# Kernel optimization log

Hardware: AMD Instinct MI355X
Metric: run time of the kernel (lower is better)

## Reference

```python
import jax, jax.numpy as jnp
import numpy as np

B, S, H = 2, 1024, 2048          # batch, seq, hidden_size
I = 7168                          # intermediate_size
E = 8                             # num_local_experts
TOPK = 2                          # num_experts_per_tok
R = int(I * H * 0.1 / (I + H))    # delta_low_rank = 159


def setup_inputs() -> dict:
    key = jax.random.key(0)
    ks = jax.random.split(key, 12)
    s = 0.02
    return {
        "hidden_states": jax.random.normal(ks[0], (B, S, H), jnp.float32),
        "gate_w": jax.random.normal(ks[1], (E, H), jnp.float32) * s,
        "W1": jax.random.normal(ks[2], (E, I, H), jnp.float32) * s,
        "W2": jax.random.normal(ks[3], (E, H, I), jnp.float32) * s,
        "W3": jax.random.normal(ks[4], (E, I, H), jnp.float32) * s,
        "U1": jax.random.normal(ks[5], (E, I, R), jnp.float32) * s,
        "V1": jax.random.normal(ks[6], (E, R, H), jnp.float32) * s,
        "U2": jax.random.normal(ks[7], (E, H, R), jnp.float32) * s,
        "V2": jax.random.normal(ks[8], (E, R, I), jnp.float32) * s,
        "U3": jax.random.normal(ks[9], (E, I, R), jnp.float32) * s,
        "V3": jax.random.normal(ks[10], (E, R, H), jnp.float32) * s,
    }


def reference(hidden_states, gate_w, W1, W2, W3, U1, V1, U2, V2, U3, V3):
    b, s, h = hidden_states.shape
    x = hidden_states.reshape(-1, h)                     # [T, H]
    T = x.shape[0]
    router_logits = x @ gate_w.T                          # [T, E]
    probs = jax.nn.softmax(router_logits.astype(jnp.float32), axis=-1)
    rw, sel = jax.lax.top_k(probs, TOPK)                  # [T, k]
    rw = rw / jnp.sum(rw, axis=-1, keepdims=True)
    rw = rw.astype(x.dtype)
    # dense combine weights: zero for unselected experts (same math as gather/scatter)
    comb = jnp.zeros((T, E), x.dtype).at[jnp.arange(T)[:, None], sel].add(rw)
    out = jnp.zeros_like(x)
    for e in range(E):                                    # small fixed expert loop
        up = x @ W3[e].T + (x @ V3[e].T) @ U3[e].T        # [T, I]
        gate = x @ W1[e].T + (x @ V1[e].T) @ U1[e].T      # [T, I]
        hmid = jax.nn.silu(gate) * up                     # [T, I]
        y = hmid @ W2[e].T + (hmid @ V2[e].T) @ U2[e].T   # [T, H]
        out = out + comb[:, e, None] * y
    return out.reshape(b, s, h), router_logits
```

## Files before the change

kernel.cpp:

```cpp
#include <hip/hip_runtime.h>
#include <cstdint>
#include <cstddef>

#define TT 2048
#define HH 2048
#define II 7168
#define EE 8
#define RR 159
#define RPAD 192
#define ROWS 4096

typedef __attribute__((ext_vector_type(8))) short bf16x8;
typedef __attribute__((ext_vector_type(4))) short short4v;
typedef __attribute__((ext_vector_type(4))) float f32x4;

__device__ __forceinline__ unsigned short f2bf(float f) {
  unsigned int u = __float_as_uint(f);
  u += 0x7fffu + ((u >> 16) & 1u);
  return (unsigned short)(u >> 16);
}
__device__ __forceinline__ float bf2f(unsigned short u) {
  return __uint_as_float(((unsigned int)u) << 16);
}
__device__ __forceinline__ bf16x8 zero8() {
  bf16x8 v;
#pragma unroll
  for (int j = 0; j < 8; j++) v[j] = 0;
  return v;
}
__device__ __forceinline__ void gload16(const unsigned short* g, unsigned short* l) {
  __builtin_amdgcn_global_load_lds(
      (const __attribute__((address_space(1))) unsigned int*)g,
      (__attribute__((address_space(3))) unsigned int*)l, 16, 0, 0);
}

__global__ __launch_bounds__(256) void k_f2bf_flat(const float* __restrict__ s,
                                                   unsigned short* __restrict__ d,
                                                   long long n8) {
  long long i = (long long)blockIdx.x * blockDim.x + threadIdx.x;
  long long stride = (long long)gridDim.x * blockDim.x;
  for (; i < n8; i += stride) {
    const float* p = s + i * 8;
    float4 a = *(const float4*)p;
    float4 b = *(const float4*)(p + 4);
    bf16x8 v;
    v[0] = (short)f2bf(a.x); v[1] = (short)f2bf(a.y);
    v[2] = (short)f2bf(a.z); v[3] = (short)f2bf(a.w);
    v[4] = (short)f2bf(b.x); v[5] = (short)f2bf(b.y);
    v[6] = (short)f2bf(b.z); v[7] = (short)f2bf(b.w);
    *(bf16x8*)(d + i * 8) = v;
  }
}

__global__ __launch_bounds__(256) void k_upad(const float* __restrict__ U,
                                              unsigned short* __restrict__ Up, int rows) {
  long long idx = (long long)blockIdx.x * 256 + threadIdx.x;
  long long total = (long long)rows * 24;
  if (idx >= total) return;
  int row = (int)(idx / 24), c8 = (int)(idx % 24);
  unsigned short* dp = Up + (size_t)row * RPAD + c8 * 8;
#pragma unroll
  for (int j = 0; j < 8; j++) {
    int c = c8 * 8 + j;
    dp[j] = (c < RR) ? f2bf(U[(size_t)row * RR + c]) : (unsigned short)0;
  }
}

__global__ __launch_bounds__(256, 2) void k_merge(
    const float* __restrict__ Wf, const unsigned short* __restrict__ Upad,
    const unsigned short* __restrict__ Vb, unsigned short* __restrict__ Wb,
    int M2, int C) {
  int e = blockIdx.z;
  int row0 = blockIdx.y * 128;
  int col0 = blockIdx.x * 128;
  const float* w = Wf + (size_t)e * M2 * C;
  const unsigned short* up = Upad + (size_t)e * M2 * RPAD;
  const unsigned short* vb = Vb + (size_t)e * RR * C;
  unsigned short* wb = Wb + (size_t)e * M2 * C;
  __shared__ unsigned short sbuf[17408];
  unsigned short* Us = sbuf;
  unsigned short* Vt = sbuf + 8192;
  unsigned short* Dl = sbuf;
  int tid = threadIdx.x, lane = tid & 63, wv = tid >> 6;
  int wr = (wv >> 1) * 64, wc = (wv & 1) * 64;
  int rstage = tid >> 3, cg = tid & 7;
  f32x4 acc[4][4];
#pragma unroll
  for (int m = 0; m < 4; m++)
#pragma unroll
    for (int n = 0; n < 4; n++) acc[m][n] = (f32x4){0.f, 0.f, 0.f, 0.f};
  int rl = tid & 15;
  int h8 = (tid >> 4) * 8;
  for (int kt = 0; kt < RPAD; kt += 64) {
#pragma unroll
    for (int p = 0; p < 4; p++) {
      int r = p * 32 + rstage;
      bf16x8 v = *(const bf16x8*)(up + (size_t)(row0 + r) * RPAD + kt + cg * 8);
      *(bf16x8*)&Us[r * 64 + ((cg ^ (r & 7)) * 8)] = v;
    }
#pragma unroll
    for (int rr = 0; rr < 4; rr++) {
      int r = rr * 16 + rl;
      int rg = kt + r;
      bf16x8 v = zero8();
      if (rg < RR) v = *(const bf16x8*)(vb + (size_t)rg * C + col0 + h8);
#pragma unroll
      for (int j = 0; j < 8; j++) Vt[(h8 + j) * 72 + r] = (unsigned short)v[j];
    }
    __syncthreads();
#pragma unroll
    for (int ks = 0; ks < 2; ks++) {
      bf16x8 af[4], bf[4];
#pragma unroll
      for (int m = 0; m < 4; m++) {
        int r = wr + m * 16 + (lane & 15);
        af[m] = *(const bf16x8*)&Us[r * 64 + (((ks * 4 + (lane >> 4)) ^ (r & 7)) * 8)];
      }
#pragma unroll
      for (int n = 0; n < 4; n++) {
        int h = wc + n * 16 + (lane & 15);
        bf[n] = *(const bf16x8*)&Vt[h * 72 + (ks * 4 + (lane >> 4)) * 8];
      }
#pragma unroll
      for (int m = 0; m < 4; m++)
#pragma unroll
        for (int n = 0; n < 4; n++)
          acc[m][n] = __builtin_amdgcn_mfma_f32_16x16x32_bf16(af[m], bf[n], acc[m][n], 0, 0, 0);
    }
    __syncthreads();
  }
#pragma unroll
  for (int m = 0; m < 4; m++) {
#pragma unroll
    for (int r4 = 0; r4 < 4; r4++) {
      int row = wr + m * 16 + (lane >> 4) * 4 + r4;
#pragma unroll
      for (int n = 0; n < 4; n++) {
        int col = wc + n * 16 + (lane & 15);
        Dl[row * 136 + col] = f2bf(acc[m][n][r4]);
      }
    }
  }
  __syncthreads();
  {
    int rr = tid >> 5;
    int c4 = (tid & 31) * 4;
#pragma unroll
    for (int pass = 0; pass < 16; pass++) {
      int row = pass * 8 + rr;
      const float* src = w + (size_t)(row0 + row) * C + col0 + c4;
      float4 a = *(const float4*)src;
      const unsigned short* dl = &Dl[row * 136 + c4];
      short4v o;
      o[0] = (short)f2bf(a.x + bf2f(dl[0]));
      o[1] = (short)f2bf(a.y + bf2f(dl[1]));
      o[2] = (short)f2bf(a.z + bf2f(dl[2]));
      o[3] = (short)f2bf(a.w + bf2f(dl[3]));
      *(short4v*)(wb + (size_t)(row0 + row) * C + col0 + c4) = o;
    }
  }
}

__global__ __launch_bounds__(256) void k_router(
    const float* __restrict__ x, const float* __restrict__ gw,
    float* __restrict__ logits_out, int* __restrict__ sel,
    float* __restrict__ wtok, int* __restrict__ counts,
    unsigned short* __restrict__ xb) {
  int t = blockIdx.x;
  const float* xr = x + (size_t)t * HH;
  int base = threadIdx.x * 8;
  float4 x0 = *(const float4*)(xr + base);
  float4 x1 = *(const float4*)(xr + base + 4);
  {
    bf16x8 v;
    v[0] = (short)f2bf(x0.x); v[1] = (short)f2bf(x0.y);
    v[2] = (short)f2bf(x0.z); v[3] = (short)f2bf(x0.w);
    v[4] = (short)f2bf(x1.x); v[5] = (short)f2bf(x1.y);
    v[6] = (short)f2bf(x1.z); v[7] = (short)f2bf(x1.w);
    *(bf16x8*)(xb + (size_t)t * HH + base) = v;
  }
  float part[EE];
#pragma unroll
  for (int e = 0; e < EE; e++) {
    const float* g = gw + (size_t)e * HH + base;
    float4 g0 = *(const float4*)g;
    float4 g1 = *(const float4*)(g + 4);
    part[e] = x0.x * g0.x + x0.y * g0.y + x0.z * g0.z + x0.w * g0.w +
              x1.x * g1.x + x1.y * g1.y + x1.z * g1.z + x1.w * g1.w;
  }
#pragma unroll
  for (int off = 32; off > 0; off >>= 1)
#pragma unroll
    for (int e = 0; e < EE; e++) part[e] += __shfl_down(part[e], off);
  __shared__ float red[4][EE];
  int w = threadIdx.x >> 6, lane = threadIdx.x & 63;
  if (lane == 0) {
#pragma unroll
    for (int e = 0; e < EE; e++) red[w][e] = part[e];
  }
  __syncthreads();
  if (threadIdx.x == 0) {
    float lg[EE];
    float mx = -1e30f;
#pragma unroll
    for (int e = 0; e < EE; e++) {
      lg[e] = red[0][e] + red[1][e] + red[2][e] + red[3][e];
      logits_out[(size_t)t * EE + e] = lg[e];
      mx = fmaxf(mx, lg[e]);
    }
    float p[EE];
#pragma unroll
    for (int e = 0; e < EE; e++) p[e] = __expf(lg[e] - mx);
    int i0 = 0;
#pragma unroll
    for (int e = 1; e < EE; e++)
      if (lg[e] > lg[i0]) i0 = e;
    int i1 = (i0 == 0) ? 1 : 0;
#pragma unroll
    for (int e = 0; e < EE; e++)
      if (e != i0 && lg[e] > lg[i1]) i1 = e;
    float s = p[i0] + p[i1];
    sel[t * 2] = i0;
    sel[t * 2 + 1] = i1;
    wtok[t * 2] = p[i0] / s;
    wtok[t * 2 + 1] = p[i1] / s;
    atomicAdd(&counts[i0], 1);
    atomicAdd(&counts[i1], 1);
  }
}

__global__ void k_offsets(const int* __restrict__ counts, int* __restrict__ offs,
                          int* __restrict__ curs) {
  if (threadIdx.x == 0 && blockIdx.x == 0) {
    int o = 0;
    for (int e = 0; e < EE; e++) {
      offs[e] = o;
      curs[e] = o;
      o += counts[e];
    }
    offs[EE] = o;
  }
}

__global__ void k_build(const int* __restrict__ sel, const float* __restrict__ wtok,
                        int* __restrict__ curs, int* __restrict__ rowsA,
                        float* __restrict__ rowwgt, int* __restrict__ rowid) {
  int t = blockIdx.x * blockDim.x + threadIdx.x;
  if (t >= TT) return;
  for (int k = 0; k < 2; k++) {
    int e = sel[t * 2 + k];
    int pos = atomicAdd(&curs[e], 1);
    rowsA[pos] = t;
    rowwgt[pos] = wtok[t * 2 + k];
    rowid[t * 2 + k] = pos;
  }
}

__global__ __launch_bounds__(256, 2) void k_mlp1(
    const unsigned short* __restrict__ Xb,
    const unsigned short* __restrict__ W1b, const unsigned short* __restrict__ W3b,
    unsigned short* __restrict__ hmid,
    const int* __restrict__ counts, const int* __restrict__ offs,
    const int* __restrict__ rowsA) {
  int e = blockIdx.z;
  int cnt = counts[e];
  int m0 = blockIdx.y * 128;
  if (m0 >= cnt) return;
  int n0 = blockIdx.x * 128;
  int roff = offs[e];
  __shared__ unsigned short As[128 * 64];
  __shared__ unsigned short Bg[128 * 64];
  __shared__ unsigned short Bu[128 * 64];
  int tid = threadIdx.x, lane = tid & 63, w = tid >> 6;
  int wr = (w >> 1) * 64, wc = (w & 1) * 64;
  f32x4 accg[4][4], accu[4][4];
#pragma unroll
  for (int m = 0; m < 4; m++)
#pragma unroll
    for (int n = 0; n < 4; n++) {
      accg[m][n] = (f32x4){0.f, 0.f, 0.f, 0.f};
      accu[m][n] = (f32x4){0.f, 0.f, 0.f, 0.f};
    }
  int srow = (w << 5) + (lane >> 3);
  int swz = (((lane & 7) ^ ((lane >> 3) & 7)) << 3);
  const unsigned short* pa[4];
  const unsigned short* pg[4];
  const unsigned short* pu[4];
  {
    const unsigned short* w1 = W1b + (size_t)e * II * HH;
    const unsigned short* w3 = W3b + (size_t)e * II * HH;
#pragma unroll
    for (int i = 0; i < 4; i++) {
      int gr = m0 + srow + i * 8;
      if (gr >= cnt) gr = cnt - 1;
      pa[i] = Xb + (size_t)rowsA[roff + gr] * HH + swz;
      pg[i] = w1 + (size_t)(n0 + srow + i * 8) * HH + swz;
      pu[i] = w3 + (size_t)(n0 + srow + i * 8) * HH + swz;
    }
  }
  for (int kt = 0; kt < HH; kt += 64) {
#pragma unroll
    for (int i = 0; i < 4; i++) {
      gload16(pa[i] + kt, &As[((w << 5) + (i << 3)) * 64]);
      gload16(pg[i] + kt, &Bg[((w << 5) + (i << 3)) * 64]);
      gload16(pu[i] + kt, &Bu[((w << 5) + (i << 3)) * 64]);
    }
    __syncthreads();
#pragma unroll
    for (int ks = 0; ks < 2; ks++) {
      bf16x8 af[4], bg[4], bu[4];
#pragma unroll
      for (int m = 0; m < 4; m++) {
        int r = wr + m * 16 + (lane & 15);
        af[m] = *(const bf16x8*)&As[r * 64 + (((ks * 4 + (lane >> 4)) ^ (r & 7)) * 8)];
      }
#pragma unroll
      for (int n = 0; n < 4; n++) {
        int r = wc + n * 16 + (lane & 15);
        int idx = r * 64 + (((ks * 4 + (lane >> 4)) ^ (r & 7)) * 8);
        bg[n] = *(const bf16x8*)&Bg[idx];
        bu[n] = *(const bf16x8*)&Bu[idx];
      }
#pragma unroll
      for (int m = 0; m < 4; m++)
#pragma unroll
        for (int n = 0; n < 4; n++) {
          accg[m][n] = __builtin_amdgcn_mfma_f32_16x16x32_bf16(af[m], bg[n], accg[m][n], 0, 0, 0);
          accu[m][n] = __builtin_amdgcn_mfma_f32_16x16x32_bf16(af[m], bu[n], accu[m][n], 0, 0, 0);
        }
    }
    __syncthreads();
  }
#pragma unroll
  for (int m = 0; m < 4; m++) {
#pragma unroll
    for (int r4 = 0; r4 < 4; r4++) {
      int row = m0 + wr + m * 16 + (lane >> 4) * 4 + r4;
      if (row < cnt) {
        size_t rb = (size_t)(roff + row) * II + n0 + wc;
#pragma unroll
        for (int n = 0; n < 4; n++) {
          float g = accg[m][n][r4], uu = accu[m][n][r4];
          float h = (g / (1.f + __expf(-g))) * uu;
          hmid[rb + n * 16 + (lane & 15)] = f2bf(h);
        }
      }
    }
  }
}

__global__ __launch_bounds__(256, 2) void k_mlp2(
    const unsigned short* __restrict__ hmid,
    const unsigned short* __restrict__ W2b,
    const float* __restrict__ rowwgt, float* __restrict__ ybuf,
    const int* __restrict__ counts, const int* __restrict__ offs) {
  int e = blockIdx.z;
  int cnt = counts[e];
  int m0 = blockIdx.y * 128;
  if (m0 >= cnt) return;
  int n0 = blockIdx.x * 128;
  int roff = offs[e];
  __shared__ unsigned short As[128 * 64];
  __shared__ unsigned short Bs[128 * 64];
  int tid = threadIdx.x, lane = tid & 63, w = tid >> 6;
  int wr = (w >> 1) * 64, wc = (w & 1) * 64;
  f32x4 acc[4][4];
#pragma unroll
  for (int m = 0; m < 4; m++)
#pragma unroll
    for (int n = 0; n < 4; n++) acc[m][n] = (f32x4){0.f, 0.f, 0.f, 0.f};
  int srow = (w << 5) + (lane >> 3);
  int swz = (((lane & 7) ^ ((lane >> 3) & 7)) << 3);
  const unsigned short* pa[4];
  const unsigned short* pb[4];
  {
    const unsigned short* w2 = W2b + (size_t)e * HH * II;
#pragma unroll
    for (int i = 0; i < 4; i++) {
      int gr = m0 + srow + i * 8;
      if (gr >= cnt) gr = cnt - 1;
      pa[i] = hmid + (size_t)(roff + gr) * II + swz;
      pb[i] = w2 + (size_t)(n0 + srow + i * 8) * II + swz;
    }
  }
  for (int kt = 0; kt < II; kt += 64) {
#pragma unroll
    for (int i = 0; i < 4; i++) {
      gload16(pa[i] + kt, &As[((w << 5) + (i << 3)) * 64]);
      gload16(pb[i] + kt, &Bs[((w << 5) + (i << 3)) * 64]);
    }
    __syncthreads();
#pragma unroll
    for (int ks = 0; ks < 2; ks++) {
      bf16x8 af[4], bs[4];
#pragma unroll
      for (int m = 0; m < 4; m++) {
        int r = wr + m * 16 + (lane & 15);
        af[m] = *(const bf16x8*)&As[r * 64 + (((ks * 4 + (lane >> 4)) ^ (r & 7)) * 8)];
      }
#pragma unroll
      for (int n = 0; n < 4; n++) {
        int r = wc + n * 16 + (lane & 15);
        bs[n] = *(const bf16x8*)&Bs[r * 64 + (((ks * 4 + (lane >> 4)) ^ (r & 7)) * 8)];
      }
#pragma unroll
      for (int m = 0; m < 4; m++)
#pragma unroll
        for (int n = 0; n < 4; n++)
          acc[m][n] = __builtin_amdgcn_mfma_f32_16x16x32_bf16(af[m], bs[n], acc[m][n], 0, 0, 0);
    }
    __syncthreads();
  }
#pragma unroll
  for (int m = 0; m < 4; m++) {
#pragma unroll
    for (int r4 = 0; r4 < 4; r4++) {
      int row = m0 + wr + m * 16 + (lane >> 4) * 4 + r4;
      if (row < cnt) {
        float wgt = rowwgt[roff + row];
        size_t rb = (size_t)(roff + row) * HH + n0 + wc;
#pragma unroll
        for (int n = 0; n < 4; n++)
          ybuf[rb + n * 16 + (lane & 15)] = acc[m][n][r4] * wgt;
      }
    }
  }
}

__global__ void k_combine(const float* __restrict__ ybuf, const int* __restrict__ rowid,
                          float* __restrict__ out) {
  int idx = blockIdx.x * 256 + threadIdx.x;
  int t = idx >> 8;
  int c = (idx & 255) * 8;
  int r0 = rowid[t * 2], r1 = rowid[t * 2 + 1];
  const float* y0 = ybuf + (size_t)r0 * HH + c;
  const float* y1 = ybuf + (size_t)r1 * HH + c;
  float4 a0 = *(const float4*)y0, a1 = *(const float4*)(y0 + 4);
  float4 b0 = *(const float4*)y1, b1 = *(const float4*)(y1 + 4);
  float4 o0 = {a0.x + b0.x, a0.y + b0.y, a0.z + b0.z, a0.w + b0.w};
  float4 o1 = {a1.x + b1.x, a1.y + b1.y, a1.z + b1.z, a1.w + b1.w};
  float* o = out + (size_t)t * HH + c;
  *(float4*)o = o0;
  *(float4*)(o + 4) = o1;
}

extern "C" void kernel_launch(void* const* d_in, const int* in_sizes, int n_in,
                              void* d_out, int out_size, void* d_ws, size_t ws_size,
                              hipStream_t stream) {
  const float* x  = (const float*)d_in[0];
  const float* gw = (const float*)d_in[1];
  const float* W1 = (const float*)d_in[2];
  const float* W2 = (const float*)d_in[3];
  const float* W3 = (const float*)d_in[4];
  const float* U1 = (const float*)d_in[5];
  const float* V1 = (const float*)d_in[6];
  const float* U2 = (const float*)d_in[7];
  const float* V2 = (const float*)d_in[8];
  const float* U3 = (const float*)d_in[9];
  const float* V3 = (const float*)d_in[10];
  float* out = (float*)d_out;
  float* logits = out + (size_t)TT * HH;

  char* ws = (char*)d_ws;
  size_t off = 0;
  auto take = [&](size_t b) -> char* {
    char* p = ws + off;
    off += (b + 255) & ~(size_t)255;
    return p;
  };
  unsigned short* Xb   = (unsigned short*)take((size_t)TT * HH * 2);
  unsigned short* hmid = (unsigned short*)take((size_t)ROWS * II * 2);
  float* ybuf          = (float*)take((size_t)ROWS * HH * 4);
  int* sel             = (int*)take((size_t)TT * 2 * 4);
  float* wtok          = (float*)take((size_t)TT * 2 * 4);
  int* rowsA           = (int*)take((size_t)ROWS * 4);
  float* rowwgt        = (float*)take((size_t)ROWS * 4);
  int* rowid           = (int*)take((size_t)TT * 2 * 4);
  int* meta            = (int*)take(1024);
  int* counts  = meta;
  int* offs    = meta + 16;
  int* curs    = meta + 32;
  unsigned short* W1b = (unsigned short*)take((size_t)EE * II * HH * 2);
  unsigned short* W3b = (unsigned short*)take((size_t)EE * II * HH * 2);
  unsigned short* W2b = (unsigned short*)take((size_t)EE * HH * II * 2);
  unsigned short* V1b = (unsigned short*)take((size_t)EE * RR * HH * 2);
  unsigned short* V3b = (unsigned short*)take((size_t)EE * RR * HH * 2);
  unsigned short* V2b = (unsigned short*)take((size_t)EE * RR * II * 2);
  unsigned short* U1p = (unsigned short*)take((size_t)EE * II * RPAD * 2);
  unsigned short* U3p = (unsigned short*)take((size_t)EE * II * RPAD * 2);
  unsigned short* U2p = (unsigned short*)take((size_t)EE * HH * RPAD * 2);

  hipMemsetAsync(counts, 0, EE * sizeof(int), stream);
  k_f2bf_flat<<<1024, 256, 0, stream>>>(V1, V1b, (long long)EE * RR * HH / 8);
  k_f2bf_flat<<<1024, 256, 0, stream>>>(V3, V3b, (long long)EE * RR * HH / 8);
  k_f2bf_flat<<<1024, 256, 0, stream>>>(V2, V2b, (long long)EE * RR * II / 8);
  k_upad<<<(EE * II * 24 + 255) / 256, 256, 0, stream>>>(U1, U1p, EE * II);
  k_upad<<<(EE * II * 24 + 255) / 256, 256, 0, stream>>>(U3, U3p, EE * II);
  k_upad<<<(EE * HH * 24 + 255) / 256, 256, 0, stream>>>(U2, U2p, EE * HH);
  k_merge<<<dim3(HH / 128, II / 128, EE), 256, 0, stream>>>(W1, U1p, V1b, W1b, II, HH);
  k_merge<<<dim3(HH / 128, II / 128, EE), 256, 0, stream>>>(W3, U3p, V3b, W3b, II, HH);
  k_merge<<<dim3(II / 128, HH / 128, EE), 256, 0, stream>>>(W2, U2p, V2b, W2b, HH, II);
  k_router<<<TT, 256, 0, stream>>>(x, gw, logits, sel, wtok, counts, Xb);
  k_offsets<<<1, 64, 0, stream>>>(counts, offs, curs);
  k_build<<<TT / 256, 256, 0, stream>>>(sel, wtok, curs, rowsA, rowwgt, rowid);
  k_mlp1<<<dim3(II / 128, TT / 128, EE), 256, 0, stream>>>(
      Xb, W1b, W3b, hmid, counts, offs, rowsA);
  k_mlp2<<<dim3(HH / 128, TT / 128, EE), 256, 0, stream>>>(
      hmid, W2b, rowwgt, ybuf, counts, offs);
  k_combine<<<(TT * HH / 8) / 256, 256, 0, stream>>>(ybuf, rowid, out);
}
```

Before: 1.161 ms.

## Fuse V fp32-to-bf16 conversion into merge kernel and prefetch U via LDS DMA

Drops the three separate V conversion kernels and has k_merge read fp32 V directly, converting to bf16 while staging it into LDS. All three K-chunks of padded U are prefetched up front with global_load_lds into a triple LDS buffer, which removes per-chunk U staging. This saves the launches and the round trip through memory for bf16 V, at the cost of more LDS per block (possibly lower occupancy) and V being re-read in fp32 by every row tile.

```diff
diff --git a/kernel.cpp b/kernel.cpp
--- a/kernel.cpp
+++ b/kernel.cpp
@@ -34,24 +34,6 @@
       (__attribute__((address_space(3))) unsigned int*)l, 16, 0, 0);
 }
 
-__global__ __launch_bounds__(256) void k_f2bf_flat(const float* __restrict__ s,
-                                                   unsigned short* __restrict__ d,
-                                                   long long n8) {
-  long long i = (long long)blockIdx.x * blockDim.x + threadIdx.x;
-  long long stride = (long long)gridDim.x * blockDim.x;
-  for (; i < n8; i += stride) {
-    const float* p = s + i * 8;
-    float4 a = *(const float4*)p;
-    float4 b = *(const float4*)(p + 4);
-    bf16x8 v;
-    v[0] = (short)f2bf(a.x); v[1] = (short)f2bf(a.y);
-    v[2] = (short)f2bf(a.z); v[3] = (short)f2bf(a.w);
-    v[4] = (short)f2bf(b.x); v[5] = (short)f2bf(b.y);
-    v[6] = (short)f2bf(b.z); v[7] = (short)f2bf(b.w);
-    *(bf16x8*)(d + i * 8) = v;
-  }
-}
-
 __global__ __launch_bounds__(256) void k_upad(const float* __restrict__ U,
                                               unsigned short* __restrict__ Up, int rows) {
   long long idx = (long long)blockIdx.x * 256 + threadIdx.x;
@@ -68,53 +50,62 @@
 
 __global__ __launch_bounds__(256, 2) void k_merge(
     const float* __restrict__ Wf, const unsigned short* __restrict__ Upad,
-    const unsigned short* __restrict__ Vb, unsigned short* __restrict__ Wb,
+    const float* __restrict__ Vf, unsigned short* __restrict__ Wb,
     int M2, int C) {
   int e = blockIdx.z;
   int row0 = blockIdx.y * 128;
   int col0 = blockIdx.x * 128;
   const float* w = Wf + (size_t)e * M2 * C;
   const unsigned short* up = Upad + (size_t)e * M2 * RPAD;
-  const unsigned short* vb = Vb + (size_t)e * RR * C;
+  const float* vf = Vf + (size_t)e * RR * C;
   unsigned short* wb = Wb + (size_t)e * M2 * C;
-  __shared__ unsigned short sbuf[17408];
-  unsigned short* Us = sbuf;
-  unsigned short* Vt = sbuf + 8192;
-  unsigned short* Dl = sbuf;
+  __shared__ unsigned short Us[3][8192];
+  __shared__ unsigned short Vt[9216];
+  unsigned short* Dl = &Us[0][0];
   int tid = threadIdx.x, lane = tid & 63, wv = tid >> 6;
   int wr = (wv >> 1) * 64, wc = (wv & 1) * 64;
-  int rstage = tid >> 3, cg = tid & 7;
   f32x4 acc[4][4];
 #pragma unroll
   for (int m = 0; m < 4; m++)
 #pragma unroll
     for (int n = 0; n < 4; n++) acc[m][n] = (f32x4){0.f, 0.f, 0.f, 0.f};
+  int srow = (wv << 5) + (lane >> 3);
+  int swz = (((lane & 7) ^ ((lane >> 3) & 7)) << 3);
+#pragma unroll
+  for (int c = 0; c < 3; c++)
+#pragma unroll
+    for (int i = 0; i < 4; i++)
+      gload16(up + (size_t)(row0 + srow + i * 8) * RPAD + c * 64 + swz,
+              &Us[c][((wv << 5) + (i << 3)) * 64]);
   int rl = tid & 15;
   int h8 = (tid >> 4) * 8;
-  for (int kt = 0; kt < RPAD; kt += 64) {
-#pragma unroll
-    for (int p = 0; p < 4; p++) {
-      int r = p * 32 + rstage;
-      bf16x8 v = *(const bf16x8*)(up + (size_t)(row0 + r) * RPAD + kt + cg * 8);
-      *(bf16x8*)&Us[r * 64 + ((cg ^ (r & 7)) * 8)] = v;
-    }
-#pragma unroll
-    for (int rr = 0; rr < 4; rr++) {
-      int r = rr * 16 + rl;
-      int rg = kt + r;
-      bf16x8 v = zero8();
-      if (rg < RR) v = *(const bf16x8*)(vb + (size_t)rg * C + col0 + h8);
-#pragma unroll
-      for (int j = 0; j < 8; j++) Vt[(h8 + j) * 72 + r] = (unsigned short)v[j];
-    }
-    __syncthreads();
+#pragma unroll
+  for (int rr = 0; rr < 4; rr++) {
+    int r = rr * 16 + rl;
+    int rg = r;
+    float4 a = {0, 0, 0, 0}, b = {0, 0, 0, 0};
+    if (rg < RR) {
+      a = *(const float4*)(vf + (size_t)rg * C + col0 + h8);
+      b = *(const float4*)(vf + (size_t)rg * C + col0 + h8 + 4);
+    }
+    Vt[(h8 + 0) * 72 + r] = f2bf(a.x);
+    Vt[(h8 + 1) * 72 + r] = f2bf(a.y);
+    Vt[(h8 + 2) * 72 + r] = f2bf(a.z);
+    Vt[(h8 + 3) * 72 + r] = f2bf(a.w);
+    Vt[(h8 + 4) * 72 + r] = f2bf(b.x);
+    Vt[(h8 + 5) * 72 + r] = f2bf(b.y);
+    Vt[(h8 + 6) * 72 + r] = f2bf(b.z);
+    Vt[(h8 + 7) * 72 + r] = f2bf(b.w);
+  }
+  __syncthreads();
+  for (int c = 0; c < 3; c++) {
 #pragma unroll
     for (int ks = 0; ks < 2; ks++) {
       bf16x8 af[4], bf[4];
 #pragma unroll
       for (int m = 0; m < 4; m++) {
         int r = wr + m * 16 + (lane & 15);
-        af[m] = *(const bf16x8*)&Us[r * 64 + (((ks * 4 + (lane >> 4)) ^ (r & 7)) * 8)];
+        af[m] = *(const bf16x8*)&Us[c][r * 64 + (((ks * 4 + (lane >> 4)) ^ (r & 7)) * 8)];
       }
 #pragma unroll
       for (int n = 0; n < 4; n++) {
@@ -127,8 +118,30 @@
         for (int n = 0; n < 4; n++)
           acc[m][n] = __builtin_amdgcn_mfma_f32_16x16x32_bf16(af[m], bf[n], acc[m][n], 0, 0, 0);
     }
-    __syncthreads();
-  }
+    if (c < 2) {
+      __syncthreads();
+#pragma unroll
+      for (int rr = 0; rr < 4; rr++) {
+        int r = rr * 16 + rl;
+        int rg = (c + 1) * 64 + r;
+        float4 a = {0, 0, 0, 0}, b = {0, 0, 0, 0};
+        if (rg < RR) {
+          a = *(const float4*)(vf + (size_t)rg * C + col0 + h8);
+          b = *(const float4*)(vf + (size_t)rg * C + col0 + h8 + 4);
+        }
+        Vt[(h8 + 0) * 72 + r] = f2bf(a.x);
+        Vt[(h8 + 1) * 72 + r] = f2bf(a.y);
+        Vt[(h8 + 2) * 72 + r] = f2bf(a.z);
+        Vt[(h8 + 3) * 72 + r] = f2bf(a.w);
+        Vt[(h8 + 4) * 72 + r] = f2bf(b.x);
+        Vt[(h8 + 5) * 72 + r] = f2bf(b.y);
+        Vt[(h8 + 6) * 72 + r] = f2bf(b.z);
+        Vt[(h8 + 7) * 72 + r] = f2bf(b.w);
+      }
+      __syncthreads();
+    }
+  }
+  __syncthreads();
 #pragma unroll
   for (int m = 0; m < 4; m++) {
 #pragma unroll
@@ -483,23 +496,17 @@
   unsigned short* W1b = (unsigned short*)take((size_t)EE * II * HH * 2);
   unsigned short* W3b = (unsigned short*)take((size_t)EE * II * HH * 2);
   unsigned short* W2b = (unsigned short*)take((size_t)EE * HH * II * 2);
-  unsigned short* V1b = (unsigned short*)take((size_t)EE * RR * HH * 2);
-  unsigned short* V3b = (unsigned short*)take((size_t)EE * RR * HH * 2);
-  unsigned short* V2b = (unsigned short*)take((size_t)EE * RR * II * 2);
   unsigned short* U1p = (unsigned short*)take((size_t)EE * II * RPAD * 2);
   unsigned short* U3p = (unsigned short*)take((size_t)EE * II * RPAD * 2);
   unsigned short* U2p = (unsigned short*)take((size_t)EE * HH * RPAD * 2);
 
   hipMemsetAsync(counts, 0, EE * sizeof(int), stream);
-  k_f2bf_flat<<<1024, 256, 0, stream>>>(V1, V1b, (long long)EE * RR * HH / 8);
-  k_f2bf_flat<<<1024, 256, 0, stream>>>(V3, V3b, (long long)EE * RR * HH / 8);
-  k_f2bf_flat<<<1024, 256, 0, stream>>>(V2, V2b, (long long)EE * RR * II / 8);
   k_upad<<<(EE * II * 24 + 255) / 256, 256, 0, stream>>>(U1, U1p, EE * II);
   k_upad<<<(EE * II * 24 + 255) / 256, 256, 0, stream>>>(U3, U3p, EE * II);
   k_upad<<<(EE * HH * 24 + 255) / 256, 256, 0, stream>>>(U2, U2p, EE * HH);
-  k_merge<<<dim3(HH / 128, II / 128, EE), 256, 0, stream>>>(W1, U1p, V1b, W1b, II, HH);
-  k_merge<<<dim3(HH / 128, II / 128, EE), 256, 0, stream>>>(W3, U3p, V3b, W3b, II, HH);
-  k_merge<<<dim3(II / 128, HH / 128, EE), 256, 0, stream>>>(W2, U2p, V2b, W2b, HH, II);
+  k_merge<<<dim3(HH / 128, II / 128, EE), 256, 0, stream>>>(W1, U1p, V1, W1b, II, HH);
+  k_merge<<<dim3(HH / 128, II / 128, EE), 256, 0, stream>>>(W3, U3p, V3, W3b, II, HH);
+  k_merge<<<dim3(II / 128, HH / 128, EE), 256, 0, stream>>>(W2, U2p, V2, W2b, HH, II);
   k_router<<<TT, 256, 0, stream>>>(x, gw, logits, sel, wtok, counts, Xb);
   k_offsets<<<1, 64, 0, stream>>>(counts, offs, curs);
   k_build<<<TT / 256, 256, 0, stream>>>(sel, wtok, curs, rowsA, rowwgt, rowid);
```

Result: slower. 1.227 ms (+5.8%).
